# Kernel optimization log

Measured on AMD Instinct MI355X. Metric: run time of the kernel, lower is better.

Reference implementation:

```python
import jax, jax.numpy as jnp
import numpy as np

D = 768
H = 8
HD = D // H
MLP = 3072
EPS = 1e-5


def _ln(x, g, b):
    mu = jnp.mean(x, axis=-1, keepdims=True)
    var = jnp.var(x, axis=-1, keepdims=True)
    return (x - mu) * jax.lax.rsqrt(var + EPS) * g + b


def setup_inputs() -> dict:
    key = jax.random.key(0)
    ks = jax.random.split(key, 20)
    B, N = 4, 2048
    s = 0.02
    inp = {
        "x": jax.random.normal(ks[0], (B, N, D), jnp.float32),
        "position_bias": jax.random.normal(ks[1], (N, N), jnp.float32),
        "wq": jax.random.normal(ks[2], (D, D), jnp.float32) * s,
        "bq": jnp.zeros((D,), jnp.float32),
        "wk": jax.random.normal(ks[3], (D, D), jnp.float32) * s,
        "bk": jnp.zeros((D,), jnp.float32),
        "wv": jax.random.normal(ks[4], (D, D), jnp.float32) * s,
        "bv": jnp.zeros((D,), jnp.float32),
        "wo": jax.random.normal(ks[5], (D, D), jnp.float32) * s,
        "bo": jnp.zeros((D,), jnp.float32),
        "g1": jnp.ones((D,), jnp.float32),
        "b1": jnp.zeros((D,), jnp.float32),
        "g2": jnp.ones((D,), jnp.float32),
        "b2": jnp.zeros((D,), jnp.float32),
        "w_ff1": jax.random.normal(ks[6], (D, MLP), jnp.float32) * s,
        "b_ff1": jnp.zeros((MLP,), jnp.float32),
        "w_ff2": jax.random.normal(ks[7], (MLP, D), jnp.float32) * s,
        "b_ff2": jnp.zeros((D,), jnp.float32),
    }
    return inp


def reference(x, position_bias, wq, bq, wk, bk, wv, bv, wo, bo, g1, b1, g2, b2, w_ff1, b_ff1, w_ff2, b_ff2):
    B, N, _ = x.shape
    scale = HD ** -0.5
    # pre-norm attention
    n1 = _ln(x, g1, b1)
    q = (n1 @ wq + bq).reshape(B, N, H, HD).transpose(0, 2, 1, 3)
    k = (n1 @ wk + bk).reshape(B, N, H, HD).transpose(0, 2, 1, 3)
    v = (n1 @ wv + bv).reshape(B, N, H, HD).transpose(0, 2, 1, 3)
    attn = jnp.einsum('bhqd,bhkd->bhqk', q, k) * scale  # [B,H,N,N]
    attn = attn + position_bias[None, None, :, :]
    attn = jax.nn.softmax(attn, axis=-1)
    out = jnp.einsum('bhqk,bhkd->bhqd', attn, v)
    out = out.transpose(0, 2, 1, 3).reshape(B, N, D)
    out = out @ wo + bo
    x = x + out
    # pre-norm GELU MLP (exact erf gelu, torch default)
    n2 = _ln(x, g2, b2)
    h = jax.nn.gelu(n2 @ w_ff1 + b_ff1, approximate=False)
    x = x + (h @ w_ff2 + b_ff2)
    return x
```

## Files before the change

kernel.cpp:

```cpp
#include <hip/hip_runtime.h>
#include <hip/hip_bf16.h>

#define D 768
#define H 8
#define HD 96
#define MLP 3072
#define NB 2048
#define BATCH 4

typedef __attribute__((ext_vector_type(8))) short short8;
typedef __attribute__((ext_vector_type(4))) short short4v;
typedef __attribute__((ext_vector_type(4))) float f32x4;
typedef __attribute__((ext_vector_type(16))) float f32x16;
typedef __attribute__((ext_vector_type(4))) int int4v;

typedef const __attribute__((address_space(1))) unsigned int gu32;
typedef __attribute__((address_space(3))) unsigned int lu32;

__device__ inline void gload16(const void* g, void* l){
  __builtin_amdgcn_global_load_lds((gu32*)g, (lu32*)l, 16, 0, 0);
}

__device__ inline short f2b(float f){
  __hip_bfloat16 h = __float2bfloat16(f);
  return *reinterpret_cast<short*>(&h);
}
__device__ inline float b2f(short s){
  return __uint_as_float(((unsigned)(unsigned short)s) << 16);
}
__device__ inline float fexp2(float x){ return __builtin_amdgcn_exp2f(x); }

__device__ inline unsigned cvtpk(float lo, float hi){
  unsigned r;
  asm volatile("v_cvt_pk_bf16_f32 %0, %1, %2" : "=v"(r) : "v"(lo), "v"(hi));
  return r;
}

__global__ __launch_bounds__(256) void wtrans(const float* __restrict__ in, short* __restrict__ out, int K, int Nc){
  __shared__ float tile[32][33];
  int bk = blockIdx.x, bn = blockIdx.y;
  int tx = threadIdx.x & 31, ty = threadIdx.x >> 5;
  #pragma unroll
  for (int i=0;i<4;++i)
    tile[ty + i*8][tx] = in[(size_t)(bk*32 + ty + i*8)*Nc + bn*32 + tx];
  __syncthreads();
  #pragma unroll
  for (int i=0;i<4;++i)
    out[(size_t)(bn*32 + ty + i*8)*K + bk*32 + tx] = f2b(tile[tx][ty + i*8]);
}

__global__ __launch_bounds__(256) void bias_cat(const float* __restrict__ bq, const float* __restrict__ bk,
                                                const float* __restrict__ bv, float* __restrict__ o){
  int i = blockIdx.x*256 + threadIdx.x;
  if (i < 768){ o[i]=bq[i]; o[768+i]=bk[i]; o[1536+i]=bv[i]; }
}

__global__ __launch_bounds__(256) void pb_reorg(const float* __restrict__ pb, short* __restrict__ pbT){
  int qt = blockIdx.x, kb = blockIdx.y;
  int t = threadIdx.x;
  int l = t >> 2;
  int vbase = (t & 3) * 8;
  int q = qt*32 + (l & 31);
  int hi = l >> 5;
  const float L2E = 1.4426950408889634f;
  short8 o;
  #pragma unroll
  for (int j=0;j<8;++j){
    int v = vbase + j;
    int r = v & 15, tile = v >> 4;
    int k = kb*64 + tile*32 + 8*(r>>2) + (r&3) + 4*hi;
    o[j] = f2b(pb[(size_t)q*NB + k] * L2E);
  }
  *(short8*)&pbT[(((size_t)(qt*32 + kb))*64 + l)*32 + vbase] = o;
}

__global__ __launch_bounds__(256) void ln_k(const float* __restrict__ X, const float* __restrict__ gg,
                                            const float* __restrict__ bb, short* __restrict__ out){
  int row = blockIdx.x, t = threadIdx.x;
  const float* x = X + (size_t)row*D;
  float v0=x[t], v1=x[t+256], v2=x[t+512];
  float s=v0+v1+v2, ss=v0*v0+v1*v1+v2*v2;
  #pragma unroll
  for (int m=1;m<64;m<<=1){ s += __shfl_xor(s,m); ss += __shfl_xor(ss,m); }
  __shared__ float red[8];
  int w=t>>6, lane=t&63;
  if (!lane){ red[w]=s; red[4+w]=ss; }
  __syncthreads();
  s = red[0]+red[1]+red[2]+red[3];
  ss = red[4]+red[5]+red[6]+red[7];
  float mu = s*(1.f/768.f);
  float inv = rsqrtf(ss*(1.f/768.f) - mu*mu + 1e-5f);
  short* o = out + (size_t)row*D;
  o[t]     = f2b((v0-mu)*inv*gg[t]     + bb[t]);
  o[t+256] = f2b((v1-mu)*inv*gg[t+256] + bb[t+256]);
  o[t+512] = f2b((v2-mu)*inv*gg[t+512] + bb[t+512]);
}

template<int MODE>
__global__ __launch_bounds__(256) void gemm_bt(
    const short* __restrict__ A, const short* __restrict__ Bt,
    const float* __restrict__ bias, const float* __restrict__ resid,
    void* __restrict__ Cout, int Nc, int K)
{
  __shared__ __align__(16) short As[128][32];
  __shared__ __align__(16) short Bs[128][32];
  int m0 = blockIdx.x*128, n0 = blockIdx.y*128;
  int t = threadIdx.x;
  int lane = t & 63, w = t >> 6;
  int wm = w >> 1, wn = w & 1;
  int r = lane & 15, g = lane >> 4;
  const short* aSrc = A  + (size_t)(m0 + (t>>2))*K + (t&3)*8;
  const short* bSrc = Bt + (size_t)(n0 + (t>>2))*K + (t&3)*8;
  char* aDst0 = (char*)As + w*1024;
  char* aDst1 = (char*)As + 4096 + w*1024;
  char* bDst0 = (char*)Bs + w*1024;
  char* bDst1 = (char*)Bs + 4096 + w*1024;
  size_t rowK64 = (size_t)64*K;
  f32x4 acc[4][4] = {};
  for (int kt=0; kt<K; kt+=32){
    gload16(aSrc + kt,          aDst0);
    gload16(aSrc + kt + rowK64, aDst1);
    gload16(bSrc + kt,          bDst0);
    gload16(bSrc + kt + rowK64, bDst1);
    __syncthreads();
    short8 af[4], bfr[4];
    #pragma unroll
    for (int i=0;i<4;++i){
      af[i]  = *(const short8*)&As[wm*64 + i*16 + r][g*8];
      bfr[i] = *(const short8*)&Bs[wn*64 + i*16 + r][g*8];
    }
    #pragma unroll
    for (int i=0;i<4;++i)
      #pragma unroll
      for (int j=0;j<4;++j)
        acc[i][j] = __builtin_amdgcn_mfma_f32_16x16x32_bf16(af[i], bfr[j], acc[i][j], 0,0,0);
    __syncthreads();
  }
  #pragma unroll
  for (int i=0;i<4;++i){
    #pragma unroll
    for (int j=0;j<4;++j){
      int col = n0 + wn*64 + j*16 + r;
      float bv = bias[col];
      #pragma unroll
      for (int q=0;q<4;++q){
        int row = m0 + wm*64 + i*16 + g*4 + q;
        size_t idx = (size_t)row*Nc + col;
        float val = acc[i][j][q] + bv;
        if constexpr (MODE==0){
          ((short*)Cout)[idx] = f2b(val);
        } else if constexpr (MODE==2){
          float ge = 0.5f*val*(1.f + erff(val*0.70710678118654752f));
          ((short*)Cout)[idx] = f2b(ge);
        }
      }
    }
  }
}

template<int MODE>
__global__ __launch_bounds__(256) void gemm64(
    const short* __restrict__ A, const short* __restrict__ Bt,
    const float* __restrict__ bias, const float* __restrict__ resid,
    void* __restrict__ Cout, int Nc, int K)
{
  __shared__ __align__(16) short As[64][32];
  __shared__ __align__(16) short Bs[128][32];
  int m0 = blockIdx.x*64, n0 = blockIdx.y*128;
  int t = threadIdx.x;
  int lane = t & 63, w = t >> 6;
  int r = lane & 15, g = lane >> 4;
  const short* aSrc = A  + (size_t)(m0 + (t>>2))*K + (t&3)*8;
  const short* bSrc = Bt + (size_t)(n0 + (t>>2))*K + (t&3)*8;
  char* aDst  = (char*)As + w*1024;
  char* bDst0 = (char*)Bs + w*1024;
  char* bDst1 = (char*)Bs + 4096 + w*1024;
  size_t rowK64 = (size_t)64*K;
  f32x4 acc[4][2] = {};
  for (int kt=0; kt<K; kt+=32){
    gload16(aSrc + kt,          aDst);
    gload16(bSrc + kt,          bDst0);
    gload16(bSrc + kt + rowK64, bDst1);
    __syncthreads();
    short8 af[4], bfr[2];
    #pragma unroll
    for (int i=0;i<4;++i) af[i] = *(const short8*)&As[i*16 + r][g*8];
    #pragma unroll
    for (int j=0;j<2;++j) bfr[j] = *(const short8*)&Bs[w*32 + j*16 + r][g*8];
    #pragma unroll
    for (int i=0;i<4;++i)
      #pragma unroll
      for (int j=0;j<2;++j)
        acc[i][j] = __builtin_amdgcn_mfma_f32_16x16x32_bf16(af[i], bfr[j], acc[i][j], 0,0,0);
    __syncthreads();
  }
  #pragma unroll
  for (int i=0;i<4;++i){
    #pragma unroll
    for (int j=0;j<2;++j){
      int col = n0 + w*32 + j*16 + r;
      #pragma unroll
      for (int q=0;q<4;++q){
        int row = m0 + i*16 + g*4 + q;
        if constexpr (MODE==1){
          size_t idx = (size_t)row*Nc + col;
          ((float*)Cout)[idx] = acc[i][j][q] + bias[col] + resid[idx];
        } else {
          int hh = row / 96, hd = row - hh*96;
          int bb = col >> 11, nn = col & 2047;
          size_t idx = ((size_t)((bb*8 + hh)*96 + hd))*2048 + nn;
          ((short*)Cout)[idx] = f2b(acc[i][j][q] + bias[row]);
        }
      }
    }
  }
}

__global__ __launch_bounds__(256, 3) void attn_k(const short* __restrict__ qkv, const short* __restrict__ v_t,
                                                 const short* __restrict__ pbT, short* __restrict__ aout){
  int bx = blockIdx.x;
  int h = bx & 7, b = (bx>>3)&3, qb = bx>>5;
  int t = threadIdx.x, l = t & 63, w = t >> 6;
  int l31 = l & 31, hi = l >> 5, l7 = l & 7;
  __shared__ __align__(16) short Ks[2][64][128];
  __shared__ __align__(16) short Vs[96][64];
  const float SCALE2 = 0.10206207261596575f * 1.4426950408889634f;

  int qRow = qb*128 + w*32 + l31;
  const short* qg = qkv + (size_t)(b*NB + qRow)*1536 + h*HD;
  short8 qa[6];
  #pragma unroll
  for (int ds=0; ds<6; ++ds)
    qa[ds] = *(const short8*)&qg[ds*16 + hi*8];

  f32x16 oacc[3] = {};
  float m_run = -3.0e38f, l_run = 0.f;

  int kr[3], kc[3], ldsK[3];
  #pragma unroll
  for (int i=0;i<3;++i){
    int s = i*256 + t;
    kr[i] = s/12; kc[i] = s%12;
    ldsK[i] = kr[i]*128 + (kc[i] ^ (kr[i]&7))*8;
  }
  const short* kgB = qkv + (size_t)(b*NB)*1536 + 768 + h*HD;
  const short* vgB = v_t + (size_t)((b*H+h)*HD)*NB;
  const short* vsrc[3];
  char* vdst[3];
  #pragma unroll
  for (int i=0;i<3;++i){
    int s = i*256 + t;
    int vr = s>>3, vc = s&7;
    vsrc[i] = vgB + (size_t)vr*NB + (vc ^ (vr&7))*8;
    vdst[i] = (char*)Vs + (i*256 + w*64)*16;
  }
  const short* pbB = pbT + (((size_t)((qb*4 + w)*32))*64 + l)*32;

  {
    short* ks0 = &Ks[0][0][0];
    #pragma unroll
    for (int i=0;i<3;++i){
      short8 ka = *(const short8*)&kgB[(size_t)kr[i]*1536 + kc[i]*8];
      *(short8*)(ks0 + ldsK[i]) = ka;
    }
  }
  __syncthreads();

  for (int kt=0; kt<32; ++kt){
    int cur = kt & 1;
    int kbase = kt*64;
    const short* pbk = pbB + kt*2048;
    short8 pbr0 = *(const short8*)&pbk[0];
    short8 pbr1 = *(const short8*)&pbk[8];
    short8 pbr2 = *(const short8*)&pbk[16];
    short8 pbr3 = *(const short8*)&pbk[24];
    #pragma unroll
    for (int i=0;i<3;++i)
      gload16(vsrc[i] + kbase, vdst[i]);
    int kb2 = (kt < 31) ? (kbase + 64) : kbase;
    short8 kra[3];
    #pragma unroll
    for (int i=0;i<3;++i)
      kra[i] = *(const short8*)&kgB[(size_t)(kb2 + kr[i])*1536 + kc[i]*8];

    f32x16 sacc[2] = {};
    __builtin_amdgcn_s_setprio(1);
    #pragma unroll
    for (int tt=0; tt<2; ++tt){
      #pragma unroll
      for (int ds=0; ds<6; ++ds){
        short8 kf = *(const short8*)&Ks[cur][tt*32 + l31][((ds*2 + hi) ^ l7)*8];
        sacc[tt] = __builtin_amdgcn_mfma_f32_32x32x16_bf16(kf, qa[ds], sacc[tt], 0,0,0);
      }
    }
    __builtin_amdgcn_s_setprio(0);

    float vals[2][16];
    #pragma unroll
    for (int tt=0; tt<2; ++tt)
      #pragma unroll
      for (int r=0; r<16; ++r){
        int v = tt*16 + r;
        short pv = (v<8)?pbr0[v]:(v<16)?pbr1[v-8]:(v<24)?pbr2[v-16]:pbr3[v-24];
        vals[tt][r] = fmaf(sacc[tt][r], SCALE2, b2f(pv));
      }
    float pm = vals[0][0];
    #pragma unroll
    for (int tt=0; tt<2; ++tt)
      #pragma unroll
      for (int r=0; r<16; ++r) pm = fmaxf(pm, vals[tt][r]);
    pm = fmaxf(pm, __shfl_xor(pm, 32));
    if (__any(pm - m_run > 8.f)){
      float mn = fmaxf(m_run, pm);
      float f = fexp2(m_run - mn);
      l_run *= f; m_run = mn;
      int fi = __float_as_int(f);
      #pragma unroll
      for (int reg=0; reg<16; ++reg){
        int q = (reg&3) + 8*(reg>>2) + 4*hi;
        float fr = __int_as_float(__builtin_amdgcn_ds_bpermute(q<<2, fi));
        oacc[0][reg] *= fr; oacc[1][reg] *= fr; oacc[2][reg] *= fr;
      }
    }
    float p[2][16];
    float rs = 0.f;
    #pragma unroll
    for (int tt=0; tt<2; ++tt)
      #pragma unroll
      for (int r=0; r<16; ++r){
        p[tt][r] = fexp2(vals[tt][r] - m_run);
        rs += p[tt][r];
      }
    rs += __shfl_xor(rs, 32);
    l_run += rs;

    short8 pa[4];
    #pragma unroll
    for (int ks=0; ks<4; ++ks){
      int tt = ks>>1;
      int rb = (ks&1)*8;
      unsigned G0a = cvtpk(p[tt][rb+0], p[tt][rb+1]);
      unsigned G0b = cvtpk(p[tt][rb+2], p[tt][rb+3]);
      unsigned G1a = cvtpk(p[tt][rb+4], p[tt][rb+5]);
      unsigned G1b = cvtpk(p[tt][rb+6], p[tt][rb+7]);
      unsigned sG0a = (unsigned)__shfl_xor((int)G0a, 32);
      unsigned sG0b = (unsigned)__shfl_xor((int)G0b, 32);
      unsigned sG1a = (unsigned)__shfl_xor((int)G1a, 32);
      unsigned sG1b = (unsigned)__shfl_xor((int)G1b, 32);
      int4v wv;
      wv[0] = hi ? (int)sG1a : (int)G0a;
      wv[1] = hi ? (int)sG1b : (int)G0b;
      wv[2] = hi ? (int)G1a  : (int)sG0a;
      wv[3] = hi ? (int)G1b  : (int)sG0b;
      pa[ks] = __builtin_bit_cast(short8, wv);
    }

    __syncthreads();

    __builtin_amdgcn_s_setprio(1);
    #pragma unroll
    for (int dt=0; dt<3; ++dt){
      #pragma unroll
      for (int ks=0; ks<4; ++ks){
        short8 vb = *(const short8*)&Vs[dt*32 + l31][((ks*2 + hi) ^ l7)*8];
        oacc[dt] = __builtin_amdgcn_mfma_f32_32x32x16_bf16(pa[ks], vb, oacc[dt], 0,0,0);
      }
    }
    __builtin_amdgcn_s_setprio(0);

    if (kt < 31){
      short* ksn = &Ks[cur^1][0][0];
      #pragma unroll
      for (int i=0;i<3;++i)
        *(short8*)(ksn + ldsK[i]) = kra[i];
      __syncthreads();
    }
  }

  float inv_self = 1.f / l_run;
  int ii = __float_as_int(inv_self);
  #pragma unroll
  for (int reg=0; reg<16; ++reg){
    int q = (reg&3) + 8*(reg>>2) + 4*hi;
    float invq = __int_as_float(__builtin_amdgcn_ds_bpermute(q<<2, ii));
    int rowg = b*NB + qb*128 + w*32 + q;
    #pragma unroll
    for (int dt=0; dt<3; ++dt){
      int col = h*HD + dt*32 + l31;
      aout[(size_t)rowg*D + col] = f2b(oacc[dt][reg] * invq);
    }
  }
}

extern "C" void kernel_launch(void* const* d_in, const int* in_sizes, int n_in,
                              void* d_out, int out_size, void* d_ws, size_t ws_size,
                              hipStream_t stream){
  const float* x   = (const float*)d_in[0];
  const float* pb  = (const float*)d_in[1];
  const float* wq  = (const float*)d_in[2];
  const float* bq  = (const float*)d_in[3];
  const float* wk  = (const float*)d_in[4];
  const float* bk  = (const float*)d_in[5];
  const float* wv  = (const float*)d_in[6];
  const float* bv  = (const float*)d_in[7];
  const float* wo  = (const float*)d_in[8];
  const float* bo  = (const float*)d_in[9];
  const float* g1  = (const float*)d_in[10];
  const float* b1  = (const float*)d_in[11];
  const float* g2  = (const float*)d_in[12];
  const float* b2  = (const float*)d_in[13];
  const float* wf1 = (const float*)d_in[14];
  const float* bf1 = (const float*)d_in[15];
  const float* wf2 = (const float*)d_in[16];
  const float* bf2 = (const float*)d_in[17];
  float* out = (float*)d_out;

  char* p = (char*)d_ws;
  auto alloc = [&](size_t bytes){ char* q = p; p += (bytes + 255) & ~(size_t)255; return q; };
  short* wqkv_t = (short*)alloc((size_t)2304*768*2);
  short* wo_t   = (short*)alloc((size_t)768*768*2);
  short* w1_t   = (short*)alloc((size_t)3072*768*2);
  short* w2_t   = (short*)alloc((size_t)768*3072*2);
  float* bqkv   = (float*)alloc(2304*4);
  short* pbT    = (short*)alloc((size_t)2048*2048*2);
  float* x1     = (float*)alloc((size_t)8192*768*4);
  short* n2     = (short*)alloc((size_t)8192*768*2);
  short* n1     = (short*)alloc((size_t)8192*768*2);
  short* qkv    = (short*)alloc((size_t)8192*1536*2);
  short* v_t    = (short*)alloc((size_t)32*96*2048*2);
  short* hbuf   = n1;
  short* attn_o = n1;
  short* wv_t   = wqkv_t + (size_t)2*768*768;

  wtrans<<<dim3(24,24),256,0,stream>>>(wq, wqkv_t,           768, 768);
  wtrans<<<dim3(24,24),256,0,stream>>>(wk, wqkv_t + 768*768, 768, 768);
  wtrans<<<dim3(24,24),256,0,stream>>>(wv, wv_t,             768, 768);
  wtrans<<<dim3(24,24),256,0,stream>>>(wo, wo_t, 768, 768);
  wtrans<<<dim3(24,96),256,0,stream>>>(wf1, w1_t, 768, 3072);
  wtrans<<<dim3(96,24),256,0,stream>>>(wf2, w2_t, 3072, 768);
  bias_cat<<<3,256,0,stream>>>(bq,bk,bv,bqkv);
  pb_reorg<<<dim3(64,32),256,0,stream>>>(pb, pbT);
  ln_k<<<8192,256,0,stream>>>(x, g1, b1, n1);
  gemm_bt<0><<<dim3(64,12),256,0,stream>>>(n1, wqkv_t, bqkv, nullptr, qkv, 1536, 768);
  gemm64<5><<<dim3(12,64),256,0,stream>>>(wv_t, n1, bv, nullptr, v_t, 0, 768);
  attn_k<<<512,256,0,stream>>>(qkv, v_t, pbT, attn_o);
  gemm64<1><<<dim3(128,6),256,0,stream>>>(attn_o, wo_t, bo, x, x1, 768, 768);
  ln_k<<<8192,256,0,stream>>>(x1, g2, b2, n2);
  gemm_bt<2><<<dim3(64,24),256,0,stream>>>(n2, w1_t, bf1, nullptr, hbuf, 3072, 768);
  gemm64<1><<<dim3(128,6),256,0,stream>>>(hbuf, w2_t, bf2, x1, out, 768, 3072);
}
```

Measured before the change: 339.8 us.

## Split attention KV range across two wave groups with LDS merge

Doubles the attention block to 512 threads, where two groups of four waves each process half of the key range for the same 128 query rows. The partial softmax states and accumulators are merged through shared memory at the end. K loads move from register-staged double buffering to direct global-to-LDS loads, single-buffered, with a barrier before compute and another after. This raises per-block parallelism and shortens the serial loop, at the cost of losing the load/compute overlap, adding a merge step, and allowing at most one block per CU under the new launch bounds.

Measured after the change: 364.6 us. 7.3% more time.

```diff
diff --git a/kernel.cpp b/kernel.cpp
--- a/kernel.cpp
+++ b/kernel.cpp
@@ -216,17 +216,20 @@
   }
 }
 
-__global__ __launch_bounds__(256, 3) void attn_k(const short* __restrict__ qkv, const short* __restrict__ v_t,
+__global__ __launch_bounds__(512, 1) void attn_k(const short* __restrict__ qkv, const short* __restrict__ v_t,
                                                  const short* __restrict__ pbT, short* __restrict__ aout){
+  __shared__ __align__(16) char smem[57344];
   int bx = blockIdx.x;
   int h = bx & 7, b = (bx>>3)&3, qb = bx>>5;
   int t = threadIdx.x, l = t & 63, w = t >> 6;
+  int wq = w & 3, g = w >> 2;
+  int tg = t & 255;
   int l31 = l & 31, hi = l >> 5, l7 = l & 7;
-  __shared__ __align__(16) short Ks[2][64][128];
-  __shared__ __align__(16) short Vs[96][64];
+  short* Ks = (short*)(smem + g*16384);
+  short* Vs = (short*)(smem + 32768 + g*12288);
   const float SCALE2 = 0.10206207261596575f * 1.4426950408889634f;
 
-  int qRow = qb*128 + w*32 + l31;
+  int qRow = qb*128 + wq*32 + l31;
   const short* qg = qkv + (size_t)(b*NB + qRow)*1536 + h*HD;
   short8 qa[6];
   #pragma unroll
@@ -236,52 +239,41 @@
   f32x16 oacc[3] = {};
   float m_run = -3.0e38f, l_run = 0.f;
 
-  int kr[3], kc[3], ldsK[3];
-  #pragma unroll
-  for (int i=0;i<3;++i){
-    int s = i*256 + t;
-    kr[i] = s/12; kc[i] = s%12;
-    ldsK[i] = kr[i]*128 + (kc[i] ^ (kr[i]&7))*8;
-  }
   const short* kgB = qkv + (size_t)(b*NB)*1536 + 768 + h*HD;
+  const short* ksrc[4]; char* kdst[4];
+  #pragma unroll
+  for (int j=0;j<4;++j){
+    int s = j*256 + tg;
+    int r = s >> 4, c = s & 15;
+    ksrc[j] = kgB + (size_t)r*1536 + (c ^ (r&7))*8;
+    kdst[j] = (char*)Ks + j*4096 + wq*1024;
+  }
   const short* vgB = v_t + (size_t)((b*H+h)*HD)*NB;
-  const short* vsrc[3];
-  char* vdst[3];
-  #pragma unroll
-  for (int i=0;i<3;++i){
-    int s = i*256 + t;
-    int vr = s>>3, vc = s&7;
-    vsrc[i] = vgB + (size_t)vr*NB + (vc ^ (vr&7))*8;
-    vdst[i] = (char*)Vs + (i*256 + w*64)*16;
-  }
-  const short* pbB = pbT + (((size_t)((qb*4 + w)*32))*64 + l)*32;
-
-  {
-    short* ks0 = &Ks[0][0][0];
-    #pragma unroll
-    for (int i=0;i<3;++i){
-      short8 ka = *(const short8*)&kgB[(size_t)kr[i]*1536 + kc[i]*8];
-      *(short8*)(ks0 + ldsK[i]) = ka;
-    }
-  }
-  __syncthreads();
-
-  for (int kt=0; kt<32; ++kt){
-    int cur = kt & 1;
+  const short* vsrc[3]; char* vdst[3];
+  #pragma unroll
+  for (int j=0;j<3;++j){
+    int s = j*256 + tg;
+    int vr = s >> 3, vc = s & 7;
+    vsrc[j] = vgB + (size_t)vr*NB + (vc ^ (vr&7))*8;
+    vdst[j] = (char*)Vs + j*4096 + wq*1024;
+  }
+  const short* pbB = pbT + (((size_t)((qb*4 + wq)*32))*64 + l)*32;
+
+  for (int it=0; it<16; ++it){
+    int kt = g*16 + it;
     int kbase = kt*64;
-    const short* pbk = pbB + kt*2048;
+    #pragma unroll
+    for (int j=0;j<4;++j)
+      gload16(ksrc[j] + (size_t)kbase*1536, kdst[j]);
+    #pragma unroll
+    for (int j=0;j<3;++j)
+      gload16(vsrc[j] + kbase, vdst[j]);
+    const short* pbk = pbB + (size_t)kt*2048;
     short8 pbr0 = *(const short8*)&pbk[0];
     short8 pbr1 = *(const short8*)&pbk[8];
     short8 pbr2 = *(const short8*)&pbk[16];
     short8 pbr3 = *(const short8*)&pbk[24];
-    #pragma unroll
-    for (int i=0;i<3;++i)
-      gload16(vsrc[i] + kbase, vdst[i]);
-    int kb2 = (kt < 31) ? (kbase + 64) : kbase;
-    short8 kra[3];
-    #pragma unroll
-    for (int i=0;i<3;++i)
-      kra[i] = *(const short8*)&kgB[(size_t)(kb2 + kr[i])*1536 + kc[i]*8];
+    __syncthreads();
 
     f32x16 sacc[2] = {};
     __builtin_amdgcn_s_setprio(1);
@@ -289,7 +281,7 @@
     for (int tt=0; tt<2; ++tt){
       #pragma unroll
       for (int ds=0; ds<6; ++ds){
-        short8 kf = *(const short8*)&Ks[cur][tt*32 + l31][((ds*2 + hi) ^ l7)*8];
+        short8 kf = *(const short8*)&Ks[(tt*32 + l31)*128 + (((ds*2 + hi) ^ l7)*8)];
         sacc[tt] = __builtin_amdgcn_mfma_f32_32x32x16_bf16(kf, qa[ds], sacc[tt], 0,0,0);
       }
     }
@@ -355,39 +347,52 @@
       pa[ks] = __builtin_bit_cast(short8, wv);
     }
 
-    __syncthreads();
-
     __builtin_amdgcn_s_setprio(1);
     #pragma unroll
     for (int dt=0; dt<3; ++dt){
       #pragma unroll
       for (int ks=0; ks<4; ++ks){
-        short8 vb = *(const short8*)&Vs[dt*32 + l31][((ks*2 + hi) ^ l7)*8];
+        short8 vb = *(const short8*)&Vs[(dt*32 + l31)*64 + (((ks*2 + hi) ^ l7)*8)];
         oacc[dt] = __builtin_amdgcn_mfma_f32_32x32x16_bf16(pa[ks], vb, oacc[dt], 0,0,0);
       }
     }
     __builtin_amdgcn_s_setprio(0);
 
-    if (kt < 31){
-      short* ksn = &Ks[cur^1][0][0];
-      #pragma unroll
-      for (int i=0;i<3;++i)
-        *(short8*)(ksn + ldsK[i]) = kra[i];
-      __syncthreads();
-    }
-  }
-
-  float inv_self = 1.f / l_run;
-  int ii = __float_as_int(inv_self);
-  #pragma unroll
-  for (int reg=0; reg<16; ++reg){
-    int q = (reg&3) + 8*(reg>>2) + 4*hi;
-    float invq = __int_as_float(__builtin_amdgcn_ds_bpermute(q<<2, ii));
-    int rowg = b*NB + qb*128 + w*32 + q;
-    #pragma unroll
-    for (int dt=0; dt<3; ++dt){
-      int col = h*HD + dt*32 + l31;
-      aout[(size_t)rowg*D + col] = f2b(oacc[dt][reg] * invq);
+    __syncthreads();
+  }
+
+  float* mbuf = (float*)smem;
+  if (g == 1){
+    float* myb = mbuf + (size_t)tg*52;
+    myb[0] = m_run; myb[1] = l_run;
+    #pragma unroll
+    for (int dt=0; dt<3; ++dt)
+      #pragma unroll
+      for (int r=0; r<16; ++r)
+        myb[2 + dt*16 + r] = oacc[dt][r];
+  }
+  __syncthreads();
+  if (g == 0){
+    const float* ob = mbuf + (size_t)tg*52;
+    float mB = ob[0], lB = ob[1];
+    float mF = fmaxf(m_run, mB);
+    float fA = fexp2(m_run - mF);
+    float fB = fexp2(mB - mF);
+    float linv = 1.f / (fA*l_run + fB*lB);
+    int iA = __float_as_int(fA), iB = __float_as_int(fB), iL = __float_as_int(linv);
+    #pragma unroll
+    for (int reg=0; reg<16; ++reg){
+      int q = (reg&3) + 8*(reg>>2) + 4*hi;
+      float fAq = __int_as_float(__builtin_amdgcn_ds_bpermute(q<<2, iA));
+      float fBq = __int_as_float(__builtin_amdgcn_ds_bpermute(q<<2, iB));
+      float lq  = __int_as_float(__builtin_amdgcn_ds_bpermute(q<<2, iL));
+      int rowg = b*NB + qb*128 + wq*32 + q;
+      #pragma unroll
+      for (int dt=0; dt<3; ++dt){
+        int col = h*HD + dt*32 + l31;
+        float vB = ob[2 + dt*16 + reg];
+        aout[(size_t)rowg*D + col] = f2b((fAq*oacc[dt][reg] + fBq*vB) * lq);
+      }
     }
   }
 }
@@ -443,7 +448,7 @@
   ln_k<<<8192,256,0,stream>>>(x, g1, b1, n1);
   gemm_bt<0><<<dim3(64,12),256,0,stream>>>(n1, wqkv_t, bqkv, nullptr, qkv, 1536, 768);
   gemm64<5><<<dim3(12,64),256,0,stream>>>(wv_t, n1, bv, nullptr, v_t, 0, 768);
-  attn_k<<<512,256,0,stream>>>(qkv, v_t, pbT, attn_o);
+  attn_k<<<512,512,0,stream>>>(qkv, v_t, pbT, attn_o);
   gemm64<1><<<dim3(128,6),256,0,stream>>>(attn_o, wo_t, bo, x, x1, 768, 768);
   ln_k<<<8192,256,0,stream>>>(x1, g2, b2, n2);
   gemm_bt<2><<<dim3(64,24),256,0,stream>>>(n2, w1_t, bf1, nullptr, hbuf, 3072, 768);
```
